# Optimization experiments

Measured on AMD Instinct MI355X. Metric: run time of the kernel, lower is better.

The kernel has to match this reference:

```python
import jax, jax.numpy as jnp
from jax import lax
import numpy as np

B, H, W, C = 8, 128, 128, 256
NUM_ANCHORS_PER_LOC = 15  # len(scales)=5 * len(ratios)=3


def _conv(x, w, b, padding):
    # NHWC conv, HWIO kernel (matches keras Conv2D)
    y = lax.conv_general_dilated(x, w, window_strides=(1, 1), padding=padding,
                                 dimension_numbers=('NHWC', 'HWIO', 'NHWC'))
    return y + b


def setup_inputs() -> dict:
    key = jax.random.key(0)
    ks = jax.random.split(key, 5)
    std = jnp.float32(0.01)  # TruncatedNormal(0, 0.01) init in original
    x = jax.random.normal(ks[0], (B, H, W, C), jnp.float32)
    w_shared = jax.random.normal(ks[1], (3, 3, C, 512), jnp.float32) * std
    b_shared = jnp.zeros((512,), jnp.float32)
    w_cls = jax.random.normal(ks[2], (1, 1, 512, 2 * NUM_ANCHORS_PER_LOC), jnp.float32) * std
    b_cls = jnp.zeros((2 * NUM_ANCHORS_PER_LOC,), jnp.float32)
    w_reg = jax.random.normal(ks[3], (1, 1, 512, 4 * NUM_ANCHORS_PER_LOC), jnp.float32) * std
    b_reg = jnp.zeros((4 * NUM_ANCHORS_PER_LOC,), jnp.float32)
    return {'x': x, 'w_shared': w_shared, 'b_shared': b_shared,
            'w_cls': w_cls, 'b_cls': b_cls, 'w_reg': w_reg, 'b_reg': b_reg}


def reference(x, w_shared, b_shared, w_cls, b_cls, w_reg, b_reg):
    # shared 3x3 conv + relu6
    shared = jnp.clip(_conv(x, w_shared, b_shared, 'SAME'), 0.0, 6.0)
    # class branch: 1x1 conv -> [B, num_anchors, 2] -> softmax
    cls = _conv(shared, w_cls, b_cls, 'VALID')
    rpn_class_logits = cls.reshape(cls.shape[0], -1, 2)
    rpn_probs = jax.nn.softmax(rpn_class_logits, axis=-1)
    reg = _conv(shared, w_reg, b_reg, 'VALID')
    rpn_deltas = reg.reshape(reg.shape[0], -1, 4)
    return (rpn_class_logits, rpn_probs, rpn_deltas)
```

## Files before the change

kernel.cpp:

```cpp
#include <hip/hip_runtime.h>
#include <stdint.h>


#define HH 128
#define WW 128
#define CIN 256

typedef __attribute__((ext_vector_type(8))) short short8;
typedef __attribute__((ext_vector_type(4))) float f32x4;

#define LDS_B_OFF 66560
#define LDS_TOTAL 132096

static __device__ __forceinline__ unsigned short f2bf(float f) {
    uint32_t u = __float_as_uint(f);
    uint32_t r = (u + 0x7FFFu + ((u >> 16) & 1u)) >> 16;
    return (unsigned short)r;
}

__global__ __launch_bounds__(256) void prep_wk(const float* __restrict__ w,
                                               unsigned short* __restrict__ wk) {
    __shared__ unsigned short t[32][130];
    const int c = blockIdx.x >> 2, nh = blockIdx.x & 3;
    const int dydx = c >> 3, kc = c & 7;
    #pragma unroll
    for (int e = 0; e < 16; ++e) {
        int idx = e * 256 + threadIdx.x;
        int kk = idx >> 7, n0 = idx & 127;
        float v = w[((size_t)(dydx * 256 + kc * 32 + kk)) * 512 + nh * 128 + n0];
        t[kk][n0] = f2bf(v);
    }
    __syncthreads();
    #pragma unroll
    for (int e = 0; e < 16; ++e) {
        int idx = e * 256 + threadIdx.x;
        int n0 = idx >> 5, kk = idx & 31;
        wk[(size_t)c * 16384 + (size_t)(nh * 128 + n0) * 32 + kk] = t[kk][n0];
    }
}

__global__ __launch_bounds__(256) void prep_wbr(const float* __restrict__ wc,
                                                const float* __restrict__ wr,
                                                unsigned short* __restrict__ wbr) {
    int t = blockIdx.x * 256 + threadIdx.x;
    int n = t >> 9, k = t & 511;
    float v = 0.f;
    if (n < 30) v = wc[k * 30 + n];
    else if (n >= 32 && n < 92) v = wr[k * 60 + (n - 32)];
    wbr[n * 512 + k] = f2bf(v);
}

__global__ __launch_bounds__(512, 2) void rpn_fused(
    const float* __restrict__ x, const unsigned short* __restrict__ wk,
    const float* __restrict__ bsh, const unsigned short* __restrict__ wbr,
    const float* __restrict__ bcls, const float* __restrict__ breg,
    float* __restrict__ out)
{
    extern __shared__ char smem[];
    const int tid = threadIdx.x;
    const int lane = tid & 63;
    const int wid = tid >> 6;
    const int wm = wid >> 2, wn = wid & 3;
    const int l15 = lane & 15, l4 = lane >> 4;
    const int blk = blockIdx.x;
    const int bb = blk >> 7, h = blk & 127;

    f32x4 acc[4][8];
    #pragma unroll
    for (int i = 0; i < 4; ++i)
        #pragma unroll
        for (int j = 0; j < 8; ++j) acc[i][j] = (f32x4){0.f, 0.f, 0.f, 0.f};

    {
        const char* src = reinterpret_cast<const char*>(wk) + tid * 16;
        char* dst = smem + LDS_B_OFF + tid * 16;
        #pragma unroll
        for (int r = 0; r < 4; ++r)
            __builtin_amdgcn_global_load_lds(
                reinterpret_cast<const uint32_t*>(src + r * 8192),
                reinterpret_cast<uint32_t*>(dst + r * 8192), 16, 0, 0);
    }

    int g = 0;
    for (int dy = 0; dy < 3; ++dy) {
        {
            const int hp = h + dy - 1;
            const bool hin = (hp >= 0) && (hp < HH);
            const float* xrow = x + ((size_t)(bb * HH + hp)) * WW * CIN;
            for (int u = tid; u < 130 * 32; u += 512) {
                const int pos = u >> 5, c8 = u & 31;
                const int wc = pos - 1;
                float4 f0 = make_float4(0.f,0.f,0.f,0.f), f1 = make_float4(0.f,0.f,0.f,0.f);
                if (hin && (unsigned)wc < WW) {
                    const float4* p = reinterpret_cast<const float4*>(xrow + (size_t)wc * CIN + c8 * 8);
                    f0 = p[0]; f1 = p[1];
                }
                short8 v;
                v[0]=(short)f2bf(f0.x); v[1]=(short)f2bf(f0.y);
                v[2]=(short)f2bf(f0.z); v[3]=(short)f2bf(f0.w);
                v[4]=(short)f2bf(f1.x); v[5]=(short)f2bf(f1.y);
                v[6]=(short)f2bf(f1.z); v[7]=(short)f2bf(f1.w);
                *reinterpret_cast<short8*>(smem + pos * 512 + ((c8 * 16) ^ ((pos & 7) << 4))) = v;
            }
        }
        for (int i = 0; i < 24; ++i, ++g) {
            const int nxt = g + 1;
            if (nxt < 72) {
                const char* src = reinterpret_cast<const char*>(wk) + (size_t)nxt * 32768 + tid * 16;
                char* dst = smem + LDS_B_OFF + ((nxt & 1) << 15) + tid * 16;
                #pragma unroll
                for (int r = 0; r < 4; ++r)
                    __builtin_amdgcn_global_load_lds(
                        reinterpret_cast<const uint32_t*>(src + r * 8192),
                        reinterpret_cast<uint32_t*>(dst + r * 8192), 16, 0, 0);
                if (i == 0) asm volatile("s_waitcnt vmcnt(4) lgkmcnt(0)" ::: "memory");
                else        asm volatile("s_waitcnt vmcnt(4)" ::: "memory");
            } else {
                asm volatile("s_waitcnt vmcnt(0) lgkmcnt(0)" ::: "memory");
            }
            __builtin_amdgcn_s_barrier();
            asm volatile("" ::: "memory");

            const int dx = (g >> 3) % 3;
            const int kc = g & 7;
            const char* bbuf = smem + LDS_B_OFF + ((g & 1) << 15);

            short8 af[4];
            const int ch = kc * 32 + l4 * 8;
            #pragma unroll
            for (int mf = 0; mf < 4; ++mf) {
                const int row = wm * 64 + mf * 16 + l15 + dx;
                af[mf] = *reinterpret_cast<const short8*>(
                    smem + row * 512 + ((ch * 2) ^ ((row & 7) << 4)));
            }
            short8 bf[8];
            #pragma unroll
            for (int nf = 0; nf < 8; ++nf) {
                const int n = wn * 128 + nf * 16 + l15;
                bf[nf] = *reinterpret_cast<const short8*>(bbuf + n * 64 + l4 * 16);
            }
            asm volatile("s_waitcnt lgkmcnt(0)" ::: "memory");
            __builtin_amdgcn_s_setprio(1);
            #pragma unroll
            for (int nf = 0; nf < 8; ++nf)
                #pragma unroll
                for (int mf = 0; mf < 4; ++mf)
                    acc[mf][nf] = __builtin_amdgcn_mfma_f32_16x16x32_bf16(
                        af[mf], bf[nf], acc[mf][nf], 0, 0, 0);
            __builtin_amdgcn_s_setprio(0);
            __builtin_amdgcn_s_barrier();
            asm volatile("" ::: "memory");
        }
    }

    __syncthreads();
    #pragma unroll
    for (int nf = 0; nf < 8; ++nf) {
        const int ch = wn * 128 + nf * 16 + l15;
        const float bv = bsh[ch];
        #pragma unroll
        for (int mf = 0; mf < 4; ++mf) {
            #pragma unroll
            for (int r = 0; r < 4; ++r) {
                const int pos = wm * 64 + mf * 16 + l4 * 4 + r;
                float v = acc[mf][nf][r] + bv;
                v = fminf(fmaxf(v, 0.f), 6.f);
                *reinterpret_cast<unsigned short*>(
                    smem + pos * 1024 + ((ch * 2) ^ ((pos & 7) << 4))) = f2bf(v);
            }
        }
    }
    __syncthreads();

    f32x4 bacc[6];
    #pragma unroll
    for (int nf = 0; nf < 6; ++nf) bacc[nf] = (f32x4){0.f,0.f,0.f,0.f};
    const int pos0 = wid * 16;
    #pragma unroll 4
    for (int kstep = 0; kstep < 16; ++kstep) {
        const int ch = kstep * 32 + l4 * 8;
        const int posr = pos0 + l15;
        short8 af = *reinterpret_cast<const short8*>(
            smem + posr * 1024 + ((ch * 2) ^ ((posr & 7) << 4)));
        #pragma unroll
        for (int nf = 0; nf < 6; ++nf) {
            const int n = nf * 16 + l15;
            short8 bfr = *reinterpret_cast<const short8*>(wbr + n * 512 + ch);
            bacc[nf] = __builtin_amdgcn_mfma_f32_16x16x32_bf16(af, bfr, bacc[nf], 0, 0, 0);
        }
    }

    const size_t rowbase = (size_t)h * 128;
    #pragma unroll
    for (int nf = 0; nf < 2; ++nf) {
        const int n = nf * 16 + l15;
        const float bias = (n < 30) ? bcls[n] : 0.f;
        #pragma unroll
        for (int r = 0; r < 4; ++r) {
            float v = bacc[nf][r] + bias;
            float vo = __shfl_xor(v, 1);
            float mx = fmaxf(v, vo);
            float e  = __expf(v - mx), eo = __expf(vo - mx);
            float p  = e / (e + eo);
            if (n < 30) {
                const int wc = pos0 + l4 * 4 + r;
                const size_t anchor = (rowbase + wc) * 15 + (n >> 1);
                const size_t idx = (size_t)bb * 491520 + anchor * 2 + (n & 1);
                out[idx] = v;
                out[3932160 + idx] = p;
            }
        }
    }
    #pragma unroll
    for (int nf = 2; nf < 6; ++nf) {
        const int n = nf * 16 + l15;
        const int nr = n - 32;
        const float bias = (nr < 60) ? breg[nr] : 0.f;
        #pragma unroll
        for (int r = 0; r < 4; ++r) {
            float v = bacc[nf][r] + bias;
            if (nr < 60) {
                const int wc = pos0 + l4 * 4 + r;
                const size_t anchor = (rowbase + wc) * 15 + (nr >> 2);
                out[7864320 + (size_t)bb * 983040 + anchor * 4 + (nr & 3)] = v;
            }
        }
    }
}

extern "C" void kernel_launch(void* const* d_in, const int* in_sizes, int n_in,
                              void* d_out, int out_size, void* d_ws, size_t ws_size,
                              hipStream_t stream) {
    const float* x    = (const float*)d_in[0];
    const float* wsh  = (const float*)d_in[1];
    const float* bsh  = (const float*)d_in[2];
    const float* wcls = (const float*)d_in[3];
    const float* bcls = (const float*)d_in[4];
    const float* wreg = (const float*)d_in[5];
    const float* breg = (const float*)d_in[6];
    float* out = (float*)d_out;

    unsigned short* wk  = (unsigned short*)d_ws;
    unsigned short* wbr = wk + 1179648;

    prep_wk <<<288, 256, 0, stream>>>(wsh, wk);
    prep_wbr<<<192, 256, 0, stream>>>(wcls, wreg, wbr);

    hipFuncSetAttribute((const void*)rpn_fused,
                        hipFuncAttributeMaxDynamicSharedMemorySize, LDS_TOTAL);
    rpn_fused<<<1024, 512, LDS_TOTAL, stream>>>(x, wk, bsh, wbr, bcls, breg, out);
}
```

Measured before the change: 616.0 us.

## Swizzle B weight layout in LDS and interleave B loads with MFMAs

The weight prep kernel now writes each 32-element K chunk with an XOR swizzle keyed on the output channel, and the main kernel reads B fragments with the matching swizzled offset. This is meant to remove LDS bank conflicts on the B fragment reads, which previously used a 64-byte row stride. The inner loop also stops preloading all eight B fragments behind an explicit lgkmcnt(0) wait. It loads each B fragment just before its four MFMAs, so LDS reads can overlap with matrix math and fewer registers are held live. The trade-off is that MFMAs may now stall on the compiler-inserted per-load waits.

```diff
diff --git a/kernel.cpp b/kernel.cpp
--- a/kernel.cpp
+++ b/kernel.cpp
@@ -35,7 +35,9 @@
     for (int e = 0; e < 16; ++e) {
         int idx = e * 256 + threadIdx.x;
         int n0 = idx >> 5, kk = idx & 31;
-        wk[(size_t)c * 16384 + (size_t)(nh * 128 + n0) * 32 + kk] = t[kk][n0];
+        int n = nh * 128 + n0;
+        int kks = kk ^ (((n >> 1) & 3) << 3);
+        wk[(size_t)c * 16384 + (size_t)n * 32 + kks] = t[kk][n0];
     }
 }
 
@@ -64,6 +66,9 @@
     const int l15 = lane & 15, l4 = lane >> 4;
     const int blk = blockIdx.x;
     const int bb = blk >> 7, h = blk & 127;
+
+    const int n0 = wn * 128 + l15;
+    const int bofs = n0 * 64 + ((l4 * 16) ^ (((n0 >> 1) & 3) << 4));
 
     f32x4 acc[4][8];
     #pragma unroll
@@ -125,28 +130,22 @@
             const int kc = g & 7;
             const char* bbuf = smem + LDS_B_OFF + ((g & 1) << 15);
 
-            short8 af[4];
-            const int ch = kc * 32 + l4 * 8;
-            #pragma unroll
-            for (int mf = 0; mf < 4; ++mf) {
-                const int row = wm * 64 + mf * 16 + l15 + dx;
-                af[mf] = *reinterpret_cast<const short8*>(
-                    smem + row * 512 + ((ch * 2) ^ ((row & 7) << 4)));
-            }
-            short8 bf[8];
+            const int r0 = wm * 64 + l15 + dx;
+            const int asw = ((kc * 32 + l4 * 8) * 2) ^ ((r0 & 7) << 4);
+            short8 af0 = *reinterpret_cast<const short8*>(smem + (r0     ) * 512 + asw);
+            short8 af1 = *reinterpret_cast<const short8*>(smem + (r0 + 16) * 512 + asw);
+            short8 af2 = *reinterpret_cast<const short8*>(smem + (r0 + 32) * 512 + asw);
+            short8 af3 = *reinterpret_cast<const short8*>(smem + (r0 + 48) * 512 + asw);
+
+            __builtin_amdgcn_s_setprio(1);
             #pragma unroll
             for (int nf = 0; nf < 8; ++nf) {
-                const int n = wn * 128 + nf * 16 + l15;
-                bf[nf] = *reinterpret_cast<const short8*>(bbuf + n * 64 + l4 * 16);
-            }
-            asm volatile("s_waitcnt lgkmcnt(0)" ::: "memory");
-            __builtin_amdgcn_s_setprio(1);
-            #pragma unroll
-            for (int nf = 0; nf < 8; ++nf)
-                #pragma unroll
-                for (int mf = 0; mf < 4; ++mf)
-                    acc[mf][nf] = __builtin_amdgcn_mfma_f32_16x16x32_bf16(
-                        af[mf], bf[nf], acc[mf][nf], 0, 0, 0);
+                short8 bfv = *reinterpret_cast<const short8*>(bbuf + bofs + nf * 1024);
+                acc[0][nf] = __builtin_amdgcn_mfma_f32_16x16x32_bf16(af0, bfv, acc[0][nf], 0, 0, 0);
+                acc[1][nf] = __builtin_amdgcn_mfma_f32_16x16x32_bf16(af1, bfv, acc[1][nf], 0, 0, 0);
+                acc[2][nf] = __builtin_amdgcn_mfma_f32_16x16x32_bf16(af2, bfv, acc[2][nf], 0, 0, 0);
+                acc[3][nf] = __builtin_amdgcn_mfma_f32_16x16x32_bf16(af3, bfv, acc[3][nf], 0, 0, 0);
+            }
             __builtin_amdgcn_s_setprio(0);
             __builtin_amdgcn_s_barrier();
             asm volatile("" ::: "memory");
```

Result: faster. 602.5 us (-2.2%).
